# Optimization experiments

Hardware: AMD Instinct MI355X
Metric: run time of the kernel (lower is better)

Reference implementation:

```python
import jax, jax.numpy as jnp
import numpy as np
from jax import lax

WS = 11
CH = 3
DENOM_G = 2 * 0.2 ** 2
DENOM_L = 2 * 0.2 ** 2
C1 = 0.01 ** 2
C2 = 0.03 ** 2


def _make_window(ws=WS, channel=CH):
    sigma = ws / 6.0
    x = np.arange(ws) - ws // 2
    g = np.exp(-(x ** 2) / (2.0 * sigma ** 2))
    g = g / g.sum()
    w2 = np.outer(g, g)  # [ws, ws]
    w = np.broadcast_to(w2, (1, channel, ws, ws)) / channel  # sum over channels, averaged
    return jnp.asarray(w, dtype=jnp.float32)


def _wconv(x, window):
    # x: [N, C, H, W] -> [N, 1, H, W], SAME padding (ws odd)
    pad = WS // 2
    return lax.conv_general_dilated(
        x, window, window_strides=(1, 1), padding=[(pad, pad), (pad, pad)],
        dimension_numbers=("NCHW", "OIHW", "NCHW"))


def setup_inputs() -> dict:
    key = jax.random.key(0)
    k1, k2 = jax.random.split(key)
    X = jax.random.uniform(k1, (1, CH, 2048, 2048), dtype=jnp.float32)
    Ys = jax.random.uniform(k2, (4, CH, 2048, 2048), dtype=jnp.float32)
    return {"X": X, "Ys": Ys}


def reference(X, Ys):
    K, C, H, W = Ys.shape
    window = _make_window(WS, C)

    muY_seq = _wconv(Ys, window).reshape(K, H, W)
    sigmaY_sq_seq = _wconv(Ys * Ys, window).reshape(K, H, W) - muY_seq * muY_seq
    patch_index = jnp.argmax(sigmaY_sq_seq, axis=0)  # [H, W]

    muX = _wconv(X, window).reshape(H, W)
    muX_sq = muX * muX
    sigmaX_sq = _wconv(X * X, window).reshape(H, W) - muX_sq
    sigmaXY = _wconv(X * Ys, window).reshape(K, H, W) - muX[None] * muY_seq

    cs_seq = (2 * sigmaXY + C2) / (sigmaX_sq[None] + sigmaY_sq_seq + C2)  # [K, H, W]
    cs_map = jnp.take_along_axis(cs_seq, patch_index[None], axis=0)[0]  # [H, W]

    # is_lum=True luminance component
    lY = jnp.mean(muY_seq.reshape(K, -1), axis=1)  # [K]
    lL = jnp.exp(-((muY_seq - 0.5) ** 2) / DENOM_L)  # [K, H, W]
    lG = jnp.exp(-((lY - 0.5) ** 2) / DENOM_G)[:, None, None]  # [K, 1, 1]
    LY = lG * lL
    muY = jnp.sum(LY * muY_seq, axis=0) / jnp.sum(LY, axis=0)  # [H, W]
    l_map = (2 * muX * muY + C1) / (muX_sq + muY * muY + C1)

    q = jnp.mean(l_map * cs_map)
    return q
```

## Files before the change

kernel.cpp:

```cpp
#include <hip/hip_runtime.h>
#include <math.h>

#define HH 2048
#define WW 2048
#define PLANE 4194304
#define PITCH 43
#define PP (26*PITCH)


__device__ inline double wave_red(double v) {
#pragma unroll
  for (int o = 32; o > 0; o >>= 1) v += __shfl_down(v, o, 64);
  return v;
}

__global__ void k0_window(float* gwin, float* gwin3) {
  if (threadIdx.x == 0) {
    double e[11], s = 0.0;
    double sig = 11.0 / 6.0;
    for (int i = 0; i < 11; ++i) {
      double x = (double)(i - 5);
      e[i] = exp(-(x * x) / (2.0 * sig * sig));
      s += e[i];
    }
    for (int i = 0; i < 11; ++i) {
      gwin[i]  = (float)(e[i] / s);
      gwin3[i] = (float)(e[i] / (3.0 * s));
    }
  }
}

__global__ __launch_bounds__(256) void k1_lY(const float* __restrict__ Ys,
                                             const float* __restrict__ gwin,
                                             double* __restrict__ lYpart) {
  int bid = blockIdx.x;
  int tid = threadIdx.x;
  double acc = 0.0;
  __shared__ float P[12];
  __shared__ double red[4];

  if (bid < 2048) {
    const float4* __restrict__ p = (const float4*)Ys;
    int base = bid * 6144 + tid;
#pragma unroll 1
    for (int gblk = 0; gblk < 3; ++gblk) {
      float ax = 0.f, ay = 0.f;
#pragma unroll
      for (int u = 0; u < 8; ++u) {
        float4 v = p[base + (gblk * 8 + u) * 256];
        ax += v.x + v.z;
        ay += v.y + v.w;
      }
      acc += (double)(ax + ay);
    }
  } else {
    int b = bid - 2048;
    int k = b >> 4, sub = b & 15;
    if (tid == 0) {
      float s = 0.f;
      for (int i = 0; i < 12; ++i) { P[i] = s; if (i < 11) s += gwin[i]; }
    }
    __syncthreads();
    const float4* __restrict__ Yk4 = (const float4*)(Ys + (size_t)k * 3 * PLANE);
    auto covP = [&](int r) -> float {
      if (r >= 5 && r <= 2042) return 1.0f;
      int dhi = r + 5; if (dhi > 10) dhi = 10;
      int dlo = r - 2042; if (dlo < 0) dlo = 0;
      return P[dhi + 1] - P[dlo];
    };
#pragma unroll 1
    for (int t = sub * 256 + tid; t < 39816; t += 4096) {
      int ch, row, g4;
      if (t < 15360) {
        ch = t / 5120;
        int r = (t % 5120) / 512;
        g4 = t & 511;
        row = (r < 5) ? r : r + 2038;
      } else {
        int u = t - 15360;
        ch = u / 8152;
        int rem = u % 8152;
        row = 5 + (rem >> 2);
        int gi = rem & 3;
        g4 = (gi < 2) ? gi : 508 + gi;
      }
      float4 v = Yk4[ch * 1048576 + row * 512 + g4];
      float cy = covP(row);
      int x0 = g4 << 2;
      float w0 = cy * covP(x0)     - 1.0f;
      float w1 = cy * covP(x0 + 1) - 1.0f;
      float w2 = cy * covP(x0 + 2) - 1.0f;
      float w3 = cy * covP(x0 + 3) - 1.0f;
      acc += (double)(w0 * v.x + w1 * v.y + w2 * v.z + w3 * v.w);
    }
  }

  acc = wave_red(acc);
  int lane = tid & 63, wid = tid >> 6;
  __syncthreads();
  if (lane == 0) red[wid] = acc;
  __syncthreads();
  if (tid == 0) {
    double tot = red[0] + red[1] + red[2] + red[3];
    if (bid < 2048) {
      int k = bid >> 9;
      lYpart[k * 528 + (bid & 511)] = tot;
    } else {
      int b = bid - 2048;
      lYpart[(b >> 4) * 528 + 512 + (b & 15)] = tot;
    }
  }
}

__global__ __launch_bounds__(256) void k2a_lG(const double* __restrict__ lYpart,
                                              double* __restrict__ lG) {
  __shared__ double red[4];
  for (int k = 0; k < 4; ++k) {
    const double* p = lYpart + k * 528;
    double v = p[threadIdx.x] + p[256 + threadIdx.x];
    if (threadIdx.x < 16) v += p[512 + threadIdx.x];
    v = wave_red(v);
    int lane = threadIdx.x & 63, wid = threadIdx.x >> 6;
    if (lane == 0) red[wid] = v;
    __syncthreads();
    if (threadIdx.x == 0) {
      double tot = red[0] + red[1] + red[2] + red[3];
      double lY = tot * (1.0 / 12582912.0);
      double d = lY - 0.5;
      lG[k] = exp(-(d * d) / 0.08);
    }
    __syncthreads();
  }
}

__global__ __launch_bounds__(512) void k2_main(const float* __restrict__ X,
                                               const float* __restrict__ Ys,
                                               const float* __restrict__ gwin,
                                               const float* __restrict__ gwin3,
                                               const double* __restrict__ lG,
                                               double* __restrict__ qpart) {
  __shared__ float prod[14 * PP];
  __shared__ double qred[8];

  int bid = blockIdx.x;
  int wg = (bid & 7) * 1024 + (bid >> 3);
  int tX = wg & 63, tY = wg >> 6;
  int x0 = tX * 32, y0 = tY * 16;
  int tid = threadIdx.x;

  float g[11], g3[11];
#pragma unroll
  for (int i = 0; i < 11; ++i) { g[i] = gwin[i]; g3[i] = gwin3[i]; }

  const size_t PL = (size_t)HH * WW;
  for (int pos = tid; pos < 42 * 26; pos += 512) {
    int py = pos / 42;
    int px = pos - py * 42;
    int gy = y0 - 5 + py;
    int gx = x0 - 5 + px;
    float xv0 = 0.f, xv1 = 0.f, xv2 = 0.f;
    float yv[12];
#pragma unroll
    for (int j = 0; j < 12; ++j) yv[j] = 0.f;
    if ((unsigned)gy < (unsigned)HH && (unsigned)gx < (unsigned)WW) {
      size_t off = (size_t)gy * WW + gx;
      xv0 = X[off];
      xv1 = X[off + PL];
      xv2 = X[off + 2 * PL];
#pragma unroll
      for (int j = 0; j < 12; ++j) yv[j] = Ys[off + (size_t)j * PL];
    }
    int o = py * PITCH + px;
    prod[0 * PP + o] = xv0 + xv1 + xv2;
    prod[1 * PP + o] = xv0 * xv0 + xv1 * xv1 + xv2 * xv2;
#pragma unroll
    for (int k = 0; k < 4; ++k) {
      float a = yv[3 * k], b = yv[3 * k + 1], c = yv[3 * k + 2];
      prod[(2 + k) * PP + o]  = a + b + c;
      prod[(6 + k) * PP + o]  = a * a + b * b + c * c;
      prod[(10 + k) * PP + o] = xv0 * a + xv1 * b + xv2 * c;
    }
  }
  __syncthreads();

#pragma unroll 1
  for (int it = 0; it < 3; ++it) {
    int t = it * 512 + tid;
    bool valid = t < 1456;
    int f = 0, py = 0, xg = 0;
    float w[18];
    if (valid) {
      f = t / 104;
      int rr = t - f * 104;
      py = rr >> 2;
      xg = (rr & 3) * 8;
      int base = f * PP + py * PITCH + xg;
#pragma unroll
      for (int j = 0; j < 18; ++j) w[j] = prod[base + j];
    }
    __syncthreads();
    if (valid) {
      int base = f * PP + py * PITCH + xg;
#pragma unroll
      for (int o = 0; o < 8; ++o) {
        float s = 0.f;
#pragma unroll
        for (int d = 0; d < 11; ++d) s += g[d] * w[o + d];
        prod[base + o] = s;
      }
    }
    __syncthreads();
  }

  if (tid < 448) {
    int f = tid >> 5, tx = tid & 31;
    int base = f * PP + tx;
    float col[26];
#pragma unroll
    for (int py = 0; py < 26; ++py) col[py] = prod[base + py * PITCH];
#pragma unroll
    for (int ty = 0; ty < 16; ++ty) {
      float s = 0.f;
#pragma unroll
      for (int d = 0; d < 11; ++d) s += g3[d] * col[ty + d];
      prod[base + ty * PITCH] = s;
    }
  }
  __syncthreads();

  {
    int ty = tid >> 5, tx = tid & 31;
    int o = ty * PITCH + tx;
    float b[14];
#pragma unroll
    for (int f = 0; f < 14; ++f) b[f] = prod[f * PP + o];
    float muX = b[0];
    float muX2 = muX * muX;
    float sigX = b[1] - muX2;
    float num = 0.f, den = 0.f;
    float best_sig = -1e30f, best_cs = 0.f;
#pragma unroll
    for (int k = 0; k < 4; ++k) {
      float muY  = b[2 + k];
      float sigY = b[6 + k] - muY * muY;
      float sXY  = b[10 + k] - muX * muY;
      float cs = (2.f * sXY + 9e-4f) / (sigX + sigY + 9e-4f);
      if (sigY > best_sig) { best_sig = sigY; best_cs = cs; }
      float dm = muY - 0.5f;
      float lL = expf(-dm * dm * 12.5f);
      float LY = (float)lG[k] * lL;
      num += LY * muY;
      den += LY;
    }
    float muYw = num / den;
    float l = (2.f * muX * muYw + 1e-4f) / (muX2 + muYw * muYw + 1e-4f);
    double v = (double)(l * best_cs);
    v = wave_red(v);
    int lane = tid & 63, wid = tid >> 6;
    if (lane == 0) qred[wid] = v;
    __syncthreads();
    if (tid == 0) {
      double t = 0.0;
#pragma unroll
      for (int i = 0; i < 8; ++i) t += qred[i];
      qpart[blockIdx.x] = t;
    }
  }
}

__global__ __launch_bounds__(512) void k3_final(const double* __restrict__ qpart,
                                                float* __restrict__ out) {
  double acc = 0.0;
  for (int i = threadIdx.x; i < 8192; i += 512) acc += qpart[i];
  acc = wave_red(acc);
  __shared__ double red[8];
  int lane = threadIdx.x & 63, wid = threadIdx.x >> 6;
  if (lane == 0) red[wid] = acc;
  __syncthreads();
  if (threadIdx.x == 0)
    out[0] = (float)((red[0] + red[1] + red[2] + red[3] +
                      red[4] + red[5] + red[6] + red[7]) * (1.0 / 4194304.0));
}

extern "C" void kernel_launch(void* const* d_in, const int* in_sizes, int n_in,
                              void* d_out, int out_size, void* d_ws, size_t ws_size,
                              hipStream_t stream) {
  const float* X  = (const float*)d_in[0];
  const float* Ys = (const float*)d_in[1];
  char* ws = (char*)d_ws;
  float*  gwin   = (float*)(ws + 0);
  float*  gwin3  = (float*)(ws + 64);
  double* lG     = (double*)(ws + 128);
  double* lYpart = (double*)(ws + 256);
  double* qpart  = (double*)(ws + 17408);
  float* out = (float*)d_out;

  hipLaunchKernelGGL(k0_window, dim3(1), dim3(64), 0, stream, gwin, gwin3);
  hipLaunchKernelGGL(k1_lY, dim3(2112), dim3(256), 0, stream, Ys, gwin, lYpart);
  hipLaunchKernelGGL(k2a_lG, dim3(1), dim3(256), 0, stream, lYpart, lG);
  hipLaunchKernelGGL(k2_main, dim3(8192), dim3(512), 0, stream, X, Ys, gwin, gwin3, lG, qpart);
  hipLaunchKernelGGL(k3_final, dim3(1), dim3(512), 0, stream, qpart, out);
}
```

Baseline: 163.5 us.

## Vectorize halo loads with float2 and run horizontal blur per row per thread

The tile-loading stage now has 286 threads each fetch 4 contiguous pixels from all 15 planes using float2 loads, replacing scalar per-pixel loads. The horizontal Gaussian pass now gives each thread a full 44-wide row and writes 32 outputs in place, which drops the three-iteration split-and-sync loop. The LDS pitch changes to 45, the separate reduction scratch is reused from the product buffer, and launch bounds now request 2 blocks per CU. These aim to cut global load instruction count and barriers, at the cost of more registers per thread and fewer active threads in the load and horizontal stages.

```diff
diff --git a/kernel.cpp b/kernel.cpp
--- a/kernel.cpp
+++ b/kernel.cpp
@@ -4,7 +4,7 @@
 #define HH 2048
 #define WW 2048
 #define PLANE 4194304
-#define PITCH 43
+#define PITCH 45
 #define PP (26*PITCH)
 
 
@@ -133,15 +133,13 @@
   }
 }
 
-__global__ __launch_bounds__(512) void k2_main(const float* __restrict__ X,
-                                               const float* __restrict__ Ys,
-                                               const float* __restrict__ gwin,
-                                               const float* __restrict__ gwin3,
-                                               const double* __restrict__ lG,
-                                               double* __restrict__ qpart) {
+__global__ __launch_bounds__(512, 2) void k2_main(const float* __restrict__ X,
+                                                  const float* __restrict__ Ys,
+                                                  const float* __restrict__ gwin,
+                                                  const float* __restrict__ gwin3,
+                                                  const double* __restrict__ lG,
+                                                  double* __restrict__ qpart) {
   __shared__ float prod[14 * PP];
-  __shared__ double qred[8];
-
   int bid = blockIdx.x;
   int wg = (bid & 7) * 1024 + (bid >> 3);
   int tX = wg & 63, tY = wg >> 6;
@@ -152,85 +150,79 @@
 #pragma unroll
   for (int i = 0; i < 11; ++i) { g[i] = gwin[i]; g3[i] = gwin3[i]; }
 
-  const size_t PL = (size_t)HH * WW;
-  for (int pos = tid; pos < 42 * 26; pos += 512) {
-    int py = pos / 42;
-    int px = pos - py * 42;
-    int gy = y0 - 5 + py;
-    int gx = x0 - 5 + px;
-    float xv0 = 0.f, xv1 = 0.f, xv2 = 0.f;
-    float yv[12];
-#pragma unroll
-    for (int j = 0; j < 12; ++j) yv[j] = 0.f;
-    if ((unsigned)gy < (unsigned)HH && (unsigned)gx < (unsigned)WW) {
-      size_t off = (size_t)gy * WW + gx;
-      xv0 = X[off];
-      xv1 = X[off + PL];
-      xv2 = X[off + 2 * PL];
-#pragma unroll
-      for (int j = 0; j < 12; ++j) yv[j] = Ys[off + (size_t)j * PL];
-    }
-    int o = py * PITCH + px;
-    prod[0 * PP + o] = xv0 + xv1 + xv2;
-    prod[1 * PP + o] = xv0 * xv0 + xv1 * xv1 + xv2 * xv2;
-#pragma unroll
-    for (int k = 0; k < 4; ++k) {
-      float a = yv[3 * k], b = yv[3 * k + 1], c = yv[3 * k + 2];
-      prod[(2 + k) * PP + o]  = a + b + c;
-      prod[(6 + k) * PP + o]  = a * a + b * b + c * c;
-      prod[(10 + k) * PP + o] = xv0 * a + xv1 * b + xv2 * c;
-    }
-  }
-  __syncthreads();
-
-#pragma unroll 1
-  for (int it = 0; it < 3; ++it) {
-    int t = it * 512 + tid;
-    bool valid = t < 1456;
-    int f = 0, py = 0, xg = 0;
-    float w[18];
-    if (valid) {
-      f = t / 104;
-      int rr = t - f * 104;
-      py = rr >> 2;
-      xg = (rr & 3) * 8;
-      int base = f * PP + py * PITCH + xg;
-#pragma unroll
-      for (int j = 0; j < 18; ++j) w[j] = prod[base + j];
-    }
-    __syncthreads();
-    if (valid) {
-      int base = f * PP + py * PITCH + xg;
-#pragma unroll
-      for (int o = 0; o < 8; ++o) {
-        float s = 0.f;
-#pragma unroll
-        for (int d = 0; d < 11; ++d) s += g[d] * w[o + d];
-        prod[base + o] = s;
-      }
-    }
-    __syncthreads();
-  }
+  if (tid < 286) {
+    int row = tid / 11, gq = tid - row * 11;
+    int gy = y0 - 5 + row;
+    int gx = x0 - 6 + 4 * gq;
+    bool rok = (unsigned)gy < (unsigned)HH;
+    size_t rb = (size_t)gy * WW;
+    float v[15][4];
+#pragma unroll
+    for (int p = 0; p < 15; ++p) {
+      const float* src = (p < 3) ? (X + (size_t)p * PLANE)
+                                 : (Ys + (size_t)(p - 3) * PLANE);
+#pragma unroll
+      for (int h = 0; h < 2; ++h) {
+        int xx = gx + 2 * h;
+        float2 t = make_float2(0.f, 0.f);
+        if (rok && (unsigned)xx < (unsigned)WW)
+          t = *(const float2*)(src + rb + xx);
+        v[p][2 * h]     = t.x;
+        v[p][2 * h + 1] = t.y;
+      }
+    }
+    int ob = row * PITCH + 4 * gq;
+#pragma unroll
+    for (int e = 0; e < 4; ++e) {
+      float xa = v[0][e], xb = v[1][e], xc = v[2][e];
+      prod[0 * PP + ob + e] = xa + xb + xc;
+      prod[1 * PP + ob + e] = xa * xa + xb * xb + xc * xc;
+#pragma unroll
+      for (int k = 0; k < 4; ++k) {
+        float ya = v[3 + 3 * k][e], yb = v[4 + 3 * k][e], yc = v[5 + 3 * k][e];
+        prod[(2 + k) * PP + ob + e]  = ya + yb + yc;
+        prod[(6 + k) * PP + ob + e]  = ya * ya + yb * yb + yc * yc;
+        prod[(10 + k) * PP + ob + e] = xa * ya + xb * yb + xc * yc;
+      }
+    }
+  }
+  __syncthreads();
+
+  if (tid < 364) {
+    int f = tid / 26, row = tid - f * 26;
+    float* rp = prod + f * PP + row * PITCH;
+    float w[44];
+#pragma unroll
+    for (int j = 0; j < 44; ++j) w[j] = rp[j];
+#pragma unroll
+    for (int c = 0; c < 32; ++c) {
+      float s = 0.f;
+#pragma unroll
+      for (int d = 0; d < 11; ++d) s += g[d] * w[c + 1 + d];
+      rp[c] = s;
+    }
+  }
+  __syncthreads();
 
   if (tid < 448) {
     int f = tid >> 5, tx = tid & 31;
-    int base = f * PP + tx;
+    float* bp = prod + f * PP + tx;
     float col[26];
 #pragma unroll
-    for (int py = 0; py < 26; ++py) col[py] = prod[base + py * PITCH];
+    for (int j = 0; j < 26; ++j) col[j] = bp[j * PITCH];
 #pragma unroll
     for (int ty = 0; ty < 16; ++ty) {
       float s = 0.f;
 #pragma unroll
       for (int d = 0; d < 11; ++d) s += g3[d] * col[ty + d];
-      prod[base + ty * PITCH] = s;
+      bp[ty * PITCH] = s;
     }
   }
   __syncthreads();
 
   {
-    int ty = tid >> 5, tx = tid & 31;
-    int o = ty * PITCH + tx;
+    int dty = tid >> 5, dtx = tid & 31;
+    int o = dty * PITCH + dtx;
     float b[14];
 #pragma unroll
     for (int f = 0; f < 14; ++f) b[f] = prod[f * PP + o];
@@ -257,13 +249,15 @@
     double v = (double)(l * best_cs);
     v = wave_red(v);
     int lane = tid & 63, wid = tid >> 6;
-    if (lane == 0) qred[wid] = v;
+    __syncthreads();
+    if (lane == 0) ((double*)prod)[wid] = v;
     __syncthreads();
     if (tid == 0) {
       double t = 0.0;
-#pragma unroll
-      for (int i = 0; i < 8; ++i) t += qred[i];
-      qpart[blockIdx.x] = t;
+      const double* qr = (const double*)prod;
+#pragma unroll
+      for (int i = 0; i < 8; ++i) t += qr[i];
+      qpart[bid] = t;
     }
   }
 }
```

Result: slower. 167.3 us (+2.3%).
